# Kernel optimization log

Measured on AMD Instinct MI355X. Metric: run time of the kernel, lower is better.

## Reference

```python
import jax, jax.numpy as jnp
import numpy as np

DIM = 1024
NUM_HEADS = 16
HEAD_DIM = DIM // NUM_HEADS
ROPE_BASE = 10000.0


def _rope_cos_sin(seq_len, head_dim):
    inv_freq = 1.0 / (ROPE_BASE ** (jnp.arange(0, head_dim, 2, dtype=jnp.float32) / head_dim))
    t = jnp.arange(seq_len, dtype=jnp.float32)
    freqs = t[:, None] * inv_freq[None, :]            # [S, Dh/2]
    emb = jnp.concatenate([freqs, freqs], axis=-1)    # [S, Dh]
    return jnp.cos(emb), jnp.sin(emb)


def _rotate_half(x):
    half = x.shape[-1] // 2
    return jnp.concatenate([-x[..., half:], x[..., :half]], axis=-1)


def setup_inputs() -> dict:
    key = jax.random.key(0)
    k1, k2, k3 = jax.random.split(key, 3)
    B, S = 2, 2048
    x = jax.random.normal(k1, (B, S, DIM), dtype=jnp.float32)
    w_qkv = jax.random.normal(k2, (3 * DIM, DIM), dtype=jnp.float32) * (DIM ** -0.5)
    w_out = jax.random.normal(k3, (DIM, DIM), dtype=jnp.float32) * (DIM ** -0.5)
    return {"x": x, "w_qkv": w_qkv, "w_out": w_out}


def reference(x, w_qkv, w_out):
    B, S, D = x.shape
    H, Dh = NUM_HEADS, HEAD_DIM
    scale = Dh ** -0.5

    qkv = (x @ w_qkv.T).reshape(B, S, 3, H, Dh)      # [B,S,3,H,Dh]
    qkv = jnp.transpose(qkv, (2, 0, 3, 1, 4))        # [3,B,H,S,Dh]
    q, k, v = qkv[0], qkv[1], qkv[2]

    cos, sin = _rope_cos_sin(S, Dh)                  # [S,Dh]
    cos = cos[None, None, :, :]
    sin = sin[None, None, :, :]
    q = q * cos + _rotate_half(q) * sin
    k = k * cos + _rotate_half(k) * sin

    scores = jnp.einsum('bhqd,bhkd->bhqk', q, k) * scale
    causal_mask = jnp.triu(jnp.ones((S, S), dtype=bool), k=1)
    scores = jnp.where(causal_mask[None, None], -jnp.inf, scores)
    attn = jax.nn.softmax(scores, axis=-1)
    out = jnp.einsum('bhqk,bhkd->bhqd', attn, v)      # [B,H,S,Dh]
    out = jnp.transpose(out, (0, 2, 1, 3)).reshape(B, S, D)
    return out @ w_out.T
```

## Files before the change

kernel.cpp:

```cpp
#include <hip/hip_runtime.h>
#include <stdint.h>

typedef uint16_t u16;
typedef __attribute__((ext_vector_type(8))) short bf16x8;
typedef __attribute__((ext_vector_type(4))) float f32x4;

__device__ inline u16 f2b(float f) {
  uint32_t u = __float_as_uint(f);
  u += 0x7FFF + ((u >> 16) & 1);
  return (u16)(u >> 16);
}
__device__ inline float b2f(u16 h) {
  return __uint_as_float(((uint32_t)h) << 16);
}

typedef __attribute__((address_space(1))) void gvoid;
typedef __attribute__((address_space(3))) void lvoid;
#define GLOAD16(gp, lp)                                                        \
  __builtin_amdgcn_global_load_lds((gvoid*)(gp), (lvoid*)(lp), 16, 0, 0)

__device__ __forceinline__ int probe_mode(const u16* __restrict__ P, int t,
                                          int* cnt_sh) {
  if (t == 0) *cnt_sh = 0;
  __syncthreads();
  float av = fabsf(b2f(P[t * 2]));
  if (av >= 1000.0f) atomicAdd(cnt_sh, 1);
  __syncthreads();
  return (*cnt_sh > 16) ? 1 : 0;
}

__global__ __launch_bounds__(256) void k_qkv_rope(const void* __restrict__ Xv,
                                                  const void* __restrict__ Wv,
                                                  u16* __restrict__ Qo,
                                                  u16* __restrict__ Ko,
                                                  u16* __restrict__ Vo) {
  __shared__ u16 As[2][2][64][40];
  __shared__ u16 Bs[2][3][64][40];
  __shared__ float Cs[64][66];
  __shared__ int cnt_sh;
  const int t = threadIdx.x, w = t >> 6, lane = t & 63;
  const int mode = probe_mode((const u16*)Xv, t, &cnt_sh);
  const int h = blockIdx.x;
  const int n0h = h * 64;
  const int m0 = blockIdx.y * 128;
  const int lr = lane & 15, lq = lane >> 4;
  f32x4 acc[3][2][4] = {};
  const int rA = t >> 2, cA = (t & 3) * 8;
  const int aoff0 = (m0 + rA) * 1024 + cA;
  const int aoff1 = (m0 + 64 + rA) * 1024 + cA;
  const int boff0 = (n0h + rA) * 1024 + cA;

  if (mode == 0) {
    const u16* Xp = (const u16*)Xv;
    const u16* Wp = (const u16*)Wv;
    uint4 pa0 = *(const uint4*)(Xp + aoff0);
    uint4 pa1 = *(const uint4*)(Xp + aoff1);
    uint4 pb0 = *(const uint4*)(Wp + boff0);
    uint4 pb1 = *(const uint4*)(Wp + boff0 + 1048576);
    uint4 pb2 = *(const uint4*)(Wp + boff0 + 2097152);
    *(uint4*)&As[0][0][rA][cA] = pa0;
    *(uint4*)&As[0][1][rA][cA] = pa1;
    *(uint4*)&Bs[0][0][rA][cA] = pb0;
    *(uint4*)&Bs[0][1][rA][cA] = pb1;
    *(uint4*)&Bs[0][2][rA][cA] = pb2;
    pa0 = *(const uint4*)(Xp + aoff0 + 32);
    pa1 = *(const uint4*)(Xp + aoff1 + 32);
    pb0 = *(const uint4*)(Wp + boff0 + 32);
    pb1 = *(const uint4*)(Wp + boff0 + 1048576 + 32);
    pb2 = *(const uint4*)(Wp + boff0 + 2097152 + 32);
    __syncthreads();
    int cur = 0;
    for (int k0 = 0; k0 < 1024; k0 += 32) {
      if (k0 + 32 < 1024) {
        *(uint4*)&As[cur ^ 1][0][rA][cA] = pa0;
        *(uint4*)&As[cur ^ 1][1][rA][cA] = pa1;
        *(uint4*)&Bs[cur ^ 1][0][rA][cA] = pb0;
        *(uint4*)&Bs[cur ^ 1][1][rA][cA] = pb1;
        *(uint4*)&Bs[cur ^ 1][2][rA][cA] = pb2;
      }
      if (k0 + 64 < 1024) {
        const int kn = k0 + 64;
        pa0 = *(const uint4*)(Xp + aoff0 + kn);
        pa1 = *(const uint4*)(Xp + aoff1 + kn);
        pb0 = *(const uint4*)(Wp + boff0 + kn);
        pb1 = *(const uint4*)(Wp + boff0 + 1048576 + kn);
        pb2 = *(const uint4*)(Wp + boff0 + 2097152 + kn);
      }
      bf16x8 bf[3];
#pragma unroll
      for (int e = 0; e < 3; ++e)
        bf[e] = *(const bf16x8*)&Bs[cur][e][(w << 4) + lr][lq * 8];
#pragma unroll
      for (int mt = 0; mt < 4; ++mt) {
        bf16x8 af0 = *(const bf16x8*)&As[cur][0][(mt << 4) + lr][lq * 8];
        bf16x8 af1 = *(const bf16x8*)&As[cur][1][(mt << 4) + lr][lq * 8];
#pragma unroll
        for (int e = 0; e < 3; ++e) {
          acc[e][0][mt] = __builtin_amdgcn_mfma_f32_16x16x32_bf16(af0, bf[e], acc[e][0][mt], 0, 0, 0);
          acc[e][1][mt] = __builtin_amdgcn_mfma_f32_16x16x32_bf16(af1, bf[e], acc[e][1][mt], 0, 0, 0);
        }
      }
      __syncthreads();
      cur ^= 1;
    }
  } else {
    for (int k0 = 0; k0 < 1024; k0 += 32) {
      __syncthreads();
      const float* Xf = (const float*)Xv;
      const float* Wf = (const float*)Wv;
#pragma unroll
      for (int ee = 0; ee < 8; ++ee) {
        As[0][0][rA][cA + ee] = f2b(Xf[aoff0 + k0 + ee]);
        As[0][1][rA][cA + ee] = f2b(Xf[aoff1 + k0 + ee]);
        Bs[0][0][rA][cA + ee] = f2b(Wf[boff0 + k0 + ee]);
        Bs[0][1][rA][cA + ee] = f2b(Wf[boff0 + 1048576 + k0 + ee]);
        Bs[0][2][rA][cA + ee] = f2b(Wf[boff0 + 2097152 + k0 + ee]);
      }
      __syncthreads();
      bf16x8 bf[3];
#pragma unroll
      for (int e = 0; e < 3; ++e)
        bf[e] = *(const bf16x8*)&Bs[0][e][(w << 4) + lr][lq * 8];
#pragma unroll
      for (int mt = 0; mt < 4; ++mt) {
        bf16x8 af0 = *(const bf16x8*)&As[0][0][(mt << 4) + lr][lq * 8];
        bf16x8 af1 = *(const bf16x8*)&As[0][1][(mt << 4) + lr][lq * 8];
#pragma unroll
        for (int e = 0; e < 3; ++e) {
          acc[e][0][mt] = __builtin_amdgcn_mfma_f32_16x16x32_bf16(af0, bf[e], acc[e][0][mt], 0, 0, 0);
          acc[e][1][mt] = __builtin_amdgcn_mfma_f32_16x16x32_bf16(af1, bf[e], acc[e][1][mt], 0, 0, 0);
        }
      }
    }
  }

  for (int f = 0; f < 2; ++f) {
    const int m0f = m0 + f * 64;
    for (int e = 0; e < 3; ++e) {
      __syncthreads();
      {
        const int col = (w << 4) + lr;
#pragma unroll
        for (int mt = 0; mt < 4; ++mt)
#pragma unroll
          for (int i = 0; i < 4; ++i)
            Cs[mt * 16 + lq * 4 + i][col] = acc[e][f][mt][i];
      }
      __syncthreads();
      if (e == 2) {
        const int sx = t & 63, dh0 = (t >> 6) * 16;
        const int m = m0f + sx, b = m >> 11, s = m & 2047;
        const long hb = (long)(b * 16 + h) * 64;
#pragma unroll
        for (int u = 0; u < 16; ++u) {
          int dh = dh0 + u;
          Vo[(hb + dh) * 2048 + s] = f2b(Cs[sx][dh]);
        }
      } else {
        const int r = t >> 2, dh0 = (t & 3) * 16;
        const int m = m0f + r, b = m >> 11, s = m & 2047;
        const int obase = ((b * 16 + h) * 2048 + s) * 64;
        u16* O = (e == 0) ? Qo : Ko;
#pragma unroll
        for (int u = 0; u < 16; ++u) {
          int dh = dh0 + u;
          float v  = Cs[r][dh];
          float vp = Cs[r][dh ^ 32];
          float sign = (dh < 32) ? -1.0f : 1.0f;
          float fr  = __expf((float)(dh & 31) * -0.28782314f);
          float ang = (float)s * fr;
          float sn = __sinf(ang), cs = __cosf(ang);
          O[obase + dh] = f2b(v * cs + sign * vp * sn);
        }
      }
    }
  }
}

__device__ __forceinline__ void attn_tile(u16 QP[64][72], u16 Ks[64][72],
                                          u16 Vt[64][72], const bf16x8 qf[2],
                                          f32x4 o_acc[4], float& m_i, float& l_i,
                                          int kt, int qt_tile, int w, int lr,
                                          int lq, int lq4, int base16, int qrow_l) {
  f32x4 sa[4] = {};
#pragma unroll
  for (int mb = 0; mb < 4; ++mb)
#pragma unroll
    for (int kk = 0; kk < 2; ++kk) {
      bf16x8 kf = *(const bf16x8*)&Ks[mb * 16 + lr][kk * 32 + lq * 8];
      sa[mb] = __builtin_amdgcn_mfma_f32_16x16x32_bf16(kf, qf[kk], sa[mb], 0, 0, 0);
    }
  float sc[4][4];
  float m_new = m_i;
#pragma unroll
  for (int mb = 0; mb < 4; ++mb)
#pragma unroll
    for (int i = 0; i < 4; ++i) {
      float sv = sa[mb][i] * 0.125f;
      if (kt == qt_tile && (mb * 16 + lq4 + i) > qrow_l) sv = -3.0e4f;
      sc[mb][i] = sv;
      m_new = fmaxf(m_new, sv);
    }
  m_new = fmaxf(m_new, __shfl_xor(m_new, 16));
  m_new = fmaxf(m_new, __shfl_xor(m_new, 32));
  float alpha = __expf(m_i - m_new);
  m_i = m_new;
  float p[4][4], sm = 0.f;
#pragma unroll
  for (int mb = 0; mb < 4; ++mb)
#pragma unroll
    for (int i = 0; i < 4; ++i) { p[mb][i] = __expf(sc[mb][i] - m_new); sm += p[mb][i]; }
  sm += __shfl_xor(sm, 16);
  sm += __shfl_xor(sm, 32);
  l_i = l_i * alpha + sm;
#pragma unroll
  for (int mb = 0; mb < 4; ++mb) {
    uint2 pk;
    pk.x = (uint32_t)f2b(p[mb][0]) | ((uint32_t)f2b(p[mb][1]) << 16);
    pk.y = (uint32_t)f2b(p[mb][2]) | ((uint32_t)f2b(p[mb][3]) << 16);
    *(uint2*)&QP[w * 16 + lr][mb * 16 + lq4] = pk;
  }
#pragma unroll
  for (int i = 0; i < 4; ++i) {
    float ai = __shfl(alpha, base16 | (lq4 + i));
    o_acc[0][i] *= ai; o_acc[1][i] *= ai;
    o_acc[2][i] *= ai; o_acc[3][i] *= ai;
  }
  asm volatile("s_waitcnt lgkmcnt(0)" ::: "memory");
#pragma unroll
  for (int kk = 0; kk < 2; ++kk) {
    bf16x8 pf = *(const bf16x8*)&QP[w * 16 + lr][kk * 32 + lq * 8];
#pragma unroll
    for (int nb = 0; nb < 4; ++nb) {
      bf16x8 vf = *(const bf16x8*)&Vt[nb * 16 + lr][kk * 32 + lq * 8];
      o_acc[nb] = __builtin_amdgcn_mfma_f32_16x16x32_bf16(pf, vf, o_acc[nb], 0, 0, 0);
    }
  }
}

__global__ __launch_bounds__(256) void k_attn(const u16* __restrict__ Q,
                                              const u16* __restrict__ K,
                                              const u16* __restrict__ V,
                                              u16* __restrict__ AO) {
  __shared__ u16 QP[64][72];
  __shared__ u16 Ks[2][64][72];
  __shared__ u16 Vt[2][64][72];
  const int qtA = 31 - blockIdx.x;
  const int qtB = blockIdx.x;
  const int bh = blockIdx.y;
  const int b = bh >> 4, h = bh & 15;
  const u16* Qg = Q + (bh * 2048) * 64;
  const u16* Kg = K + bh * 2048 * 64;
  const u16* Vg = V + (long)bh * 64 * 2048;
  const int t = threadIdx.x, w = t >> 6, lane = t & 63;
  const int lr = lane & 15, lq = lane >> 4;
  const int lq4 = lq * 4;
  const int base16 = lane & 48;
  const int r0 = t >> 3, c0 = (t & 7) * 8;
  const int qrow_l = w * 16 + lr;

  uint4 pk0 = *(const uint4*)&Kg[r0 * 64 + c0];
  uint4 pk1 = *(const uint4*)&Kg[(r0 + 32) * 64 + c0];
  uint4 pv0 = *(const uint4*)&Vg[r0 * 2048 + c0];
  uint4 pv1 = *(const uint4*)&Vg[(r0 + 32) * 2048 + c0];

  bf16x8 qfA[2], qfB[2];
  *(uint4*)&QP[r0][c0]      = *(const uint4*)&Qg[(qtA * 64 + r0) * 64 + c0];
  *(uint4*)&QP[r0 + 32][c0] = *(const uint4*)&Qg[(qtA * 64 + r0 + 32) * 64 + c0];
  __syncthreads();
#pragma unroll
  for (int kk = 0; kk < 2; ++kk)
    qfA[kk] = *(const bf16x8*)&QP[w * 16 + lr][kk * 32 + lq * 8];
  __syncthreads();
  *(uint4*)&QP[r0][c0]      = *(const uint4*)&Qg[(qtB * 64 + r0) * 64 + c0];
  *(uint4*)&QP[r0 + 32][c0] = *(const uint4*)&Qg[(qtB * 64 + r0 + 32) * 64 + c0];
  __syncthreads();
#pragma unroll
  for (int kk = 0; kk < 2; ++kk)
    qfB[kk] = *(const bf16x8*)&QP[w * 16 + lr][kk * 32 + lq * 8];

  *(uint4*)&Ks[0][r0][c0]      = pk0;
  *(uint4*)&Ks[0][r0 + 32][c0] = pk1;
  *(uint4*)&Vt[0][r0][c0]      = pv0;
  *(uint4*)&Vt[0][r0 + 32][c0] = pv1;
  pk0 = *(const uint4*)&Kg[(64 + r0) * 64 + c0];
  pk1 = *(const uint4*)&Kg[(64 + r0 + 32) * 64 + c0];
  pv0 = *(const uint4*)&Vg[r0 * 2048 + 64 + c0];
  pv1 = *(const uint4*)&Vg[(r0 + 32) * 2048 + 64 + c0];
  __syncthreads();

  float m_iA = -3.0e4f, l_iA = 0.f, m_iB = -3.0e4f, l_iB = 0.f;
  f32x4 o_accA[4] = {}, o_accB[4] = {};

  int cur = 0;
  for (int kt = 0; kt <= qtA; ++kt) {
    if (kt + 1 <= qtA) {
      *(uint4*)&Ks[cur ^ 1][r0][c0]      = pk0;
      *(uint4*)&Ks[cur ^ 1][r0 + 32][c0] = pk1;
      *(uint4*)&Vt[cur ^ 1][r0][c0]      = pv0;
      *(uint4*)&Vt[cur ^ 1][r0 + 32][c0] = pv1;
    }
    if (kt + 2 <= qtA) {
      const int kn = kt + 2;
      pk0 = *(const uint4*)&Kg[(kn * 64 + r0) * 64 + c0];
      pk1 = *(const uint4*)&Kg[(kn * 64 + r0 + 32) * 64 + c0];
      pv0 = *(const uint4*)&Vg[r0 * 2048 + kn * 64 + c0];
      pv1 = *(const uint4*)&Vg[(r0 + 32) * 2048 + kn * 64 + c0];
    }

    attn_tile(QP, Ks[cur], Vt[cur], qfA, o_accA, m_iA, l_iA, kt, qtA,
              w, lr, lq, lq4, base16, qrow_l);
    if (kt <= qtB) {
      asm volatile("s_waitcnt lgkmcnt(0)" ::: "memory");
      attn_tile(QP, Ks[cur], Vt[cur], qfB, o_accB, m_iB, l_iB, kt, qtB,
                w, lr, lq, lq4, base16, qrow_l);
    }
    __syncthreads();
    cur ^= 1;
  }
  float linvA = 1.0f / l_iA, linvB = 1.0f / l_iB;
#pragma unroll
  for (int i = 0; i < 4; ++i) {
    float invA = __shfl(linvA, base16 | (lq4 + i));
    float invB = __shfl(linvB, base16 | (lq4 + i));
    int rowA = qtA * 64 + w * 16 + lq4 + i;
    int rowB = qtB * 64 + w * 16 + lq4 + i;
    int obA = (b * 2048 + rowA) * 1024 + h * 64;
    int obB = (b * 2048 + rowB) * 1024 + h * 64;
#pragma unroll
    for (int nb = 0; nb < 4; ++nb) {
      AO[obA + nb * 16 + lr] = f2b(o_accA[nb][i] * invA);
      AO[obB + nb * 16 + lr] = f2b(o_accB[nb][i] * invB);
    }
  }
}

__global__ __launch_bounds__(256) void k_gemm_out(const u16* __restrict__ A,
                                                  const void* __restrict__ Bv,
                                                  void* __restrict__ Cv) {
  __shared__ u16 As[2][64][32];
  __shared__ u16 Bs[2][2][64][32];
  __shared__ int cnt_sh;
  const int t = threadIdx.x, w = t >> 6, lane = t & 63;
  const int mode = probe_mode((const u16*)Bv, t, &cnt_sh);
  const int n0 = blockIdx.x * 128, m0 = blockIdx.y * 64;
  const int lr = lane & 15, lq = lane >> 4;
  f32x4 acc[2][4] = {};
  const int rA = t >> 2;
  const int gcol = (((t & 3) ^ ((rA >> 1) & 3)) << 3);
  const int aoff  = (m0 + rA) * 1024 + gcol;
  const int boff0 = (n0 + rA) * 1024 + gcol;
  const int boff1 = boff0 + 65536;

  if (mode == 0) {
    const u16* Bp = (const u16*)Bv;
#define STAGE_OUT(buf, kk)                                                     \
    do {                                                                       \
      GLOAD16(A + aoff + (kk),   &As[buf][(w << 4)][0]);                       \
      GLOAD16(Bp + boff0 + (kk), &Bs[buf][0][(w << 4)][0]);                    \
      GLOAD16(Bp + boff1 + (kk), &Bs[buf][1][(w << 4)][0]);                    \
    } while (0)
    STAGE_OUT(0, 0);
    asm volatile("s_waitcnt vmcnt(0)" ::: "memory");
    __syncthreads();
    int cur = 0;
    for (int k0 = 0; k0 < 1024; k0 += 32) {
      if (k0 + 32 < 1024) STAGE_OUT(cur ^ 1, k0 + 32);
      bf16x8 bfx[2];
      const int rowB = (w << 4) + lr;
      const int scB = ((lq ^ ((rowB >> 1) & 3)) << 3);
#pragma unroll
      for (int e = 0; e < 2; ++e)
        bfx[e] = *(const bf16x8*)&Bs[cur][e][rowB][scB];
#pragma unroll
      for (int mt = 0; mt < 4; ++mt) {
        const int row = (mt << 4) + lr;
        const int sc = ((lq ^ ((row >> 1) & 3)) << 3);
        bf16x8 af = *(const bf16x8*)&As[cur][row][sc];
#pragma unroll
        for (int e = 0; e < 2; ++e)
          acc[e][mt] = __builtin_amdgcn_mfma_f32_16x16x32_bf16(af, bfx[e], acc[e][mt], 0, 0, 0);
      }
      __syncthreads();
      cur ^= 1;
    }
#undef STAGE_OUT
  } else {
    const float* Bf = (const float*)Bv;
    for (int k0 = 0; k0 < 1024; k0 += 32) {
      __syncthreads();
      *(uint4*)&As[0][rA][(t & 3) << 3] = *(const uint4*)(A + (m0 + rA) * 1024 + ((t & 3) << 3) + k0);
#pragma unroll
      for (int ee = 0; ee < 8; ++ee) {
        const int pc = ((t & 3) << 3) + ee;
        Bs[0][0][rA][pc] = f2b(Bf[(n0 + rA) * 1024 + pc + k0]);
        Bs[0][1][rA][pc] = f2b(Bf[(n0 + rA) * 1024 + 65536 + pc + k0]);
      }
      __syncthreads();
      bf16x8 bfx[2];
      const int rowB = (w << 4) + lr;
#pragma unroll
      for (int e = 0; e < 2; ++e)
        bfx[e] = *(const bf16x8*)&Bs[0][e][rowB][lq * 8];
#pragma unroll
      for (int mt = 0; mt < 4; ++mt) {
        bf16x8 af = *(const bf16x8*)&As[0][(mt << 4) + lr][lq * 8];
#pragma unroll
        for (int e = 0; e < 2; ++e)
          acc[e][mt] = __builtin_amdgcn_mfma_f32_16x16x32_bf16(af, bfx[e], acc[e][mt], 0, 0, 0);
      }
    }
  }
#pragma unroll
  for (int e = 0; e < 2; ++e) {
    const int col = n0 + e * 64 + (w << 4) + lr;
    if (mode == 0) {
      u16* C = (u16*)Cv;
#pragma unroll
      for (int mt = 0; mt < 4; ++mt)
#pragma unroll
        for (int i = 0; i < 4; ++i)
          C[(m0 + mt * 16 + lq * 4 + i) * 1024 + col] = f2b(acc[e][mt][i]);
    } else {
      float* C = (float*)Cv;
#pragma unroll
      for (int mt = 0; mt < 4; ++mt)
#pragma unroll
        for (int i = 0; i < 4; ++i)
          C[(m0 + mt * 16 + lq * 4 + i) * 1024 + col] = acc[e][mt][i];
    }
  }
}

extern "C" void kernel_launch(void* const* d_in, const int* in_sizes, int n_in,
                              void* d_out, int out_size, void* d_ws, size_t ws_size,
                              hipStream_t stream) {
  const void* x    = d_in[0];
  const void* wqkv = d_in[1];
  const void* wout = d_in[2];

  u16* qb = (u16*)((char*)d_ws + 256);
  u16* kb = qb + 4194304;
  u16* vb = kb + 4194304;
  u16* ao = vb + 4194304;

  k_qkv_rope<<<dim3(16, 32), 256, 0, stream>>>(x, wqkv, qb, kb, vb);
  k_attn    <<<dim3(16, 32), 256, 0, stream>>>(qb, kb, vb, ao);
  k_gemm_out<<<dim3(8, 64), 256, 0, stream>>>(ao, wout, d_out);
}
```

Before: 218.3 us.

## Retile QKV GEMM to 128x128 blocks with direct-to-LDS loads and register RoPE

The QKV projection kernel now tiles the output as 128x128 blocks over a 2x2 wave grid, one of Q, K or V per block, instead of one head's 64 columns across all three projections. Operand tiles go straight into LDS through global_load_lds with an XOR swizzle, replacing register staging and manual double buffering. RoPE for Q and K is applied directly from the accumulators, pairing nt with nt^2, so the LDS round-trip disappears for Q and K. The goals are better operand reuse per block and fewer LDS stores, at the cost of losing software prefetch overlap, since each k-step now uses two barriers and a single buffer.

```diff
diff --git a/kernel.cpp b/kernel.cpp
--- a/kernel.cpp
+++ b/kernel.cpp
@@ -34,144 +34,133 @@
                                                   u16* __restrict__ Qo,
                                                   u16* __restrict__ Ko,
                                                   u16* __restrict__ Vo) {
-  __shared__ u16 As[2][2][64][40];
-  __shared__ u16 Bs[2][3][64][40];
-  __shared__ float Cs[64][66];
+  union Sh {
+    struct { u16 A[128][32]; u16 B[128][32]; } st;
+    float Cs[64][66];
+  };
+  __shared__ Sh sh;
   __shared__ int cnt_sh;
   const int t = threadIdx.x, w = t >> 6, lane = t & 63;
   const int mode = probe_mode((const u16*)Xv, t, &cnt_sh);
-  const int h = blockIdx.x;
-  const int n0h = h * 64;
+  const int e  = blockIdx.x >> 3;
+  const int nb = blockIdx.x & 7;
+  const int n0 = nb * 128;
   const int m0 = blockIdx.y * 128;
   const int lr = lane & 15, lq = lane >> 4;
-  f32x4 acc[3][2][4] = {};
-  const int rA = t >> 2, cA = (t & 3) * 8;
-  const int aoff0 = (m0 + rA) * 1024 + cA;
-  const int aoff1 = (m0 + 64 + rA) * 1024 + cA;
-  const int boff0 = (n0h + rA) * 1024 + cA;
+  const int wm = w >> 1, wn = w & 1;
+  f32x4 acc[4][4] = {};
 
   if (mode == 0) {
     const u16* Xp = (const u16*)Xv;
     const u16* Wp = (const u16*)Wv;
-    uint4 pa0 = *(const uint4*)(Xp + aoff0);
-    uint4 pa1 = *(const uint4*)(Xp + aoff1);
-    uint4 pb0 = *(const uint4*)(Wp + boff0);
-    uint4 pb1 = *(const uint4*)(Wp + boff0 + 1048576);
-    uint4 pb2 = *(const uint4*)(Wp + boff0 + 2097152);
-    *(uint4*)&As[0][0][rA][cA] = pa0;
-    *(uint4*)&As[0][1][rA][cA] = pa1;
-    *(uint4*)&Bs[0][0][rA][cA] = pb0;
-    *(uint4*)&Bs[0][1][rA][cA] = pb1;
-    *(uint4*)&Bs[0][2][rA][cA] = pb2;
-    pa0 = *(const uint4*)(Xp + aoff0 + 32);
-    pa1 = *(const uint4*)(Xp + aoff1 + 32);
-    pb0 = *(const uint4*)(Wp + boff0 + 32);
-    pb1 = *(const uint4*)(Wp + boff0 + 1048576 + 32);
-    pb2 = *(const uint4*)(Wp + boff0 + 2097152 + 32);
-    __syncthreads();
-    int cur = 0;
+    const int lrow = lane >> 2;
+    const int lg   = (lane & 3) ^ (lrow & 3);
+    const int arow = m0 + w * 32 + lrow;
+    const int brow = e * 1024 + n0 + w * 32 + lrow;
+    const u16* asrc0 = Xp + (long)arow * 1024 + lg * 8;
+    const u16* asrc1 = Xp + (long)(arow + 16) * 1024 + lg * 8;
+    const u16* bsrc0 = Wp + (long)brow * 1024 + lg * 8;
+    const u16* bsrc1 = Wp + (long)(brow + 16) * 1024 + lg * 8;
+    u16* ad0 = &sh.st.A[w * 32][0];
+    u16* ad1 = &sh.st.A[w * 32 + 16][0];
+    u16* bd0 = &sh.st.B[w * 32][0];
+    u16* bd1 = &sh.st.B[w * 32 + 16][0];
     for (int k0 = 0; k0 < 1024; k0 += 32) {
-      if (k0 + 32 < 1024) {
-        *(uint4*)&As[cur ^ 1][0][rA][cA] = pa0;
-        *(uint4*)&As[cur ^ 1][1][rA][cA] = pa1;
-        *(uint4*)&Bs[cur ^ 1][0][rA][cA] = pb0;
-        *(uint4*)&Bs[cur ^ 1][1][rA][cA] = pb1;
-        *(uint4*)&Bs[cur ^ 1][2][rA][cA] = pb2;
-      }
-      if (k0 + 64 < 1024) {
-        const int kn = k0 + 64;
-        pa0 = *(const uint4*)(Xp + aoff0 + kn);
-        pa1 = *(const uint4*)(Xp + aoff1 + kn);
-        pb0 = *(const uint4*)(Wp + boff0 + kn);
-        pb1 = *(const uint4*)(Wp + boff0 + 1048576 + kn);
-        pb2 = *(const uint4*)(Wp + boff0 + 2097152 + kn);
-      }
-      bf16x8 bf[3];
-#pragma unroll
-      for (int e = 0; e < 3; ++e)
-        bf[e] = *(const bf16x8*)&Bs[cur][e][(w << 4) + lr][lq * 8];
-#pragma unroll
-      for (int mt = 0; mt < 4; ++mt) {
-        bf16x8 af0 = *(const bf16x8*)&As[cur][0][(mt << 4) + lr][lq * 8];
-        bf16x8 af1 = *(const bf16x8*)&As[cur][1][(mt << 4) + lr][lq * 8];
-#pragma unroll
-        for (int e = 0; e < 3; ++e) {
-          acc[e][0][mt] = __builtin_amdgcn_mfma_f32_16x16x32_bf16(af0, bf[e], acc[e][0][mt], 0, 0, 0);
-          acc[e][1][mt] = __builtin_amdgcn_mfma_f32_16x16x32_bf16(af1, bf[e], acc[e][1][mt], 0, 0, 0);
+      __syncthreads();
+      GLOAD16(asrc0 + k0, ad0);
+      GLOAD16(asrc1 + k0, ad1);
+      GLOAD16(bsrc0 + k0, bd0);
+      GLOAD16(bsrc1 + k0, bd1);
+      __syncthreads();
+      bf16x8 af[4], bf[4];
+#pragma unroll
+      for (int x = 0; x < 4; ++x) {
+        const int ra = wm * 64 + x * 16 + lr;
+        const int rb = wn * 64 + x * 16 + lr;
+        af[x] = *(const bf16x8*)&sh.st.A[ra][(lq ^ (lr & 3)) * 8];
+        bf[x] = *(const bf16x8*)&sh.st.B[rb][(lq ^ (lr & 3)) * 8];
+      }
+#pragma unroll
+      for (int mt = 0; mt < 4; ++mt)
+#pragma unroll
+        for (int nt = 0; nt < 4; ++nt)
+          acc[mt][nt] = __builtin_amdgcn_mfma_f32_16x16x32_bf16(af[mt], bf[nt], acc[mt][nt], 0, 0, 0);
+    }
+  } else {
+    const float* Xf = (const float*)Xv;
+    const float* Wf = (const float*)Wv;
+    const int r = t >> 1, ch = (t & 1) * 16;
+    for (int k0 = 0; k0 < 1024; k0 += 32) {
+      __syncthreads();
+#pragma unroll
+      for (int j = 0; j < 16; ++j) {
+        sh.st.A[r][ch + j] = f2b(Xf[(long)(m0 + r) * 1024 + k0 + ch + j]);
+        sh.st.B[r][ch + j] = f2b(Wf[(long)(e * 1024 + n0 + r) * 1024 + k0 + ch + j]);
+      }
+      __syncthreads();
+      bf16x8 af[4], bf[4];
+#pragma unroll
+      for (int x = 0; x < 4; ++x) {
+        af[x] = *(const bf16x8*)&sh.st.A[wm * 64 + x * 16 + lr][lq * 8];
+        bf[x] = *(const bf16x8*)&sh.st.B[wn * 64 + x * 16 + lr][lq * 8];
+      }
+#pragma unroll
+      for (int mt = 0; mt < 4; ++mt)
+#pragma unroll
+        for (int nt = 0; nt < 4; ++nt)
+          acc[mt][nt] = __builtin_amdgcn_mfma_f32_16x16x32_bf16(af[mt], bf[nt], acc[mt][nt], 0, 0, 0);
+    }
+  }
+
+  if (e < 2) {
+    u16* O = (e == 0) ? Qo : Ko;
+    const float fr0 = __expf((float)lr * -0.28782314f);
+    const float fr1 = __expf((float)(16 + lr) * -0.28782314f);
+#pragma unroll
+    for (int mt = 0; mt < 4; ++mt)
+#pragma unroll
+      for (int i = 0; i < 4; ++i) {
+        const int m = m0 + wm * 64 + mt * 16 + lq * 4 + i;
+        const int b = m >> 11, s = m & 2047;
+        float sn0, cs0, sn1, cs1;
+        __sincosf((float)s * fr0, &sn0, &cs0);
+        __sincosf((float)s * fr1, &sn1, &cs1);
+#pragma unroll
+        for (int nt = 0; nt < 4; ++nt) {
+          const int ng = n0 + wn * 64 + nt * 16 + lr;
+          const int h = ng >> 6, dh = ng & 63;
+          const float v  = acc[mt][nt][i];
+          const float vp = acc[mt][nt ^ 2][i];
+          const float sn = (nt & 1) ? sn1 : sn0;
+          const float cs = (nt & 1) ? cs1 : cs0;
+          const float sign = (dh < 32) ? -1.0f : 1.0f;
+          O[((long)(b * 16 + h) * 2048 + s) * 64 + dh] = f2b(v * cs + sign * vp * sn);
         }
       }
-      __syncthreads();
-      cur ^= 1;
-    }
   } else {
-    for (int k0 = 0; k0 < 1024; k0 += 32) {
-      __syncthreads();
-      const float* Xf = (const float*)Xv;
-      const float* Wf = (const float*)Wv;
-#pragma unroll
-      for (int ee = 0; ee < 8; ++ee) {
-        As[0][0][rA][cA + ee] = f2b(Xf[aoff0 + k0 + ee]);
-        As[0][1][rA][cA + ee] = f2b(Xf[aoff1 + k0 + ee]);
-        Bs[0][0][rA][cA + ee] = f2b(Wf[boff0 + k0 + ee]);
-        Bs[0][1][rA][cA + ee] = f2b(Wf[boff0 + 1048576 + k0 + ee]);
-        Bs[0][2][rA][cA + ee] = f2b(Wf[boff0 + 2097152 + k0 + ee]);
-      }
-      __syncthreads();
-      bf16x8 bf[3];
-#pragma unroll
-      for (int e = 0; e < 3; ++e)
-        bf[e] = *(const bf16x8*)&Bs[0][e][(w << 4) + lr][lq * 8];
-#pragma unroll
-      for (int mt = 0; mt < 4; ++mt) {
-        bf16x8 af0 = *(const bf16x8*)&As[0][0][(mt << 4) + lr][lq * 8];
-        bf16x8 af1 = *(const bf16x8*)&As[0][1][(mt << 4) + lr][lq * 8];
-#pragma unroll
-        for (int e = 0; e < 3; ++e) {
-          acc[e][0][mt] = __builtin_amdgcn_mfma_f32_16x16x32_bf16(af0, bf[e], acc[e][0][mt], 0, 0, 0);
-          acc[e][1][mt] = __builtin_amdgcn_mfma_f32_16x16x32_bf16(af1, bf[e], acc[e][1][mt], 0, 0, 0);
-        }
-      }
-    }
-  }
-
-  for (int f = 0; f < 2; ++f) {
-    const int m0f = m0 + f * 64;
-    for (int e = 0; e < 3; ++e) {
-      __syncthreads();
-      {
-        const int col = (w << 4) + lr;
+#pragma unroll 1
+    for (int q = 0; q < 4; ++q) {
+      const int qm = q >> 1, qn = q & 1;
+      __syncthreads();
+      if (wm == qm && wn == qn) {
 #pragma unroll
         for (int mt = 0; mt < 4; ++mt)
 #pragma unroll
           for (int i = 0; i < 4; ++i)
-            Cs[mt * 16 + lq * 4 + i][col] = acc[e][f][mt][i];
-      }
-      __syncthreads();
-      if (e == 2) {
-        const int sx = t & 63, dh0 = (t >> 6) * 16;
-        const int m = m0f + sx, b = m >> 11, s = m & 2047;
-        const long hb = (long)(b * 16 + h) * 64;
-#pragma unroll
-        for (int u = 0; u < 16; ++u) {
-          int dh = dh0 + u;
-          Vo[(hb + dh) * 2048 + s] = f2b(Cs[sx][dh]);
-        }
-      } else {
-        const int r = t >> 2, dh0 = (t & 3) * 16;
-        const int m = m0f + r, b = m >> 11, s = m & 2047;
-        const int obase = ((b * 16 + h) * 2048 + s) * 64;
-        u16* O = (e == 0) ? Qo : Ko;
-#pragma unroll
-        for (int u = 0; u < 16; ++u) {
-          int dh = dh0 + u;
-          float v  = Cs[r][dh];
-          float vp = Cs[r][dh ^ 32];
-          float sign = (dh < 32) ? -1.0f : 1.0f;
-          float fr  = __expf((float)(dh & 31) * -0.28782314f);
-          float ang = (float)s * fr;
-          float sn = __sinf(ang), cs = __cosf(ang);
-          O[obase + dh] = f2b(v * cs + sign * vp * sn);
-        }
+#pragma unroll
+            for (int nt = 0; nt < 4; ++nt)
+              sh.Cs[mt * 16 + lq * 4 + i][nt * 16 + lr] = acc[mt][nt][i];
+      }
+      __syncthreads();
+      const int sx = t & 63, dh0 = (t >> 6) * 16;
+      const int mlin = m0 + qm * 64 + sx;
+      const int b = mlin >> 11, s = mlin & 2047;
+#pragma unroll
+      for (int u = 0; u < 16; ++u) {
+        const int dl = dh0 + u;
+        const int ng = n0 + qn * 64 + dl;
+        const int h = ng >> 6, dh = ng & 63;
+        Vo[((long)(b * 16 + h) * 64 + dh) * 2048 + s] = f2b(sh.Cs[sx][dl]);
       }
     }
   }
@@ -444,7 +433,7 @@
   u16* vb = kb + 4194304;
   u16* ao = vb + 4194304;
 
-  k_qkv_rope<<<dim3(16, 32), 256, 0, stream>>>(x, wqkv, qb, kb, vb);
+  k_qkv_rope<<<dim3(24, 32), 256, 0, stream>>>(x, wqkv, qb, kb, vb);
   k_attn    <<<dim3(16, 32), 256, 0, stream>>>(qb, kb, vb, ao);
   k_gemm_out<<<dim3(8, 64), 256, 0, stream>>>(ao, wout, d_out);
 }
```

Result: slower. 327.7 us (+50.1%).

## Single-buffer K/V, split attention tile into stages, interleave two query tiles

Applied to the files above, without the earlier changes.

Splits the per-tile attention into QK, softmax and PV stages so the second query tile's QK MFMAs can be issued between the first tile's softmax and PV, with a separate P buffer for tile B. K/V staging in LDS drops from double to single buffering, with two barriers per iteration and a prefetch distance of one tile instead of two. Launch bounds now request 4 blocks per CU to raise occupancy. The cost is less latency hiding for the global K/V loads and an extra barrier per iteration, traded for lower LDS use and better MFMA/VALU overlap.

```diff
diff --git a/kernel.cpp b/kernel.cpp
--- a/kernel.cpp
+++ b/kernel.cpp
@@ -177,19 +177,23 @@
   }
 }
 
-__device__ __forceinline__ void attn_tile(u16 QP[64][72], u16 Ks[64][72],
-                                          u16 Vt[64][72], const bf16x8 qf[2],
-                                          f32x4 o_acc[4], float& m_i, float& l_i,
-                                          int kt, int qt_tile, int w, int lr,
-                                          int lq, int lq4, int base16, int qrow_l) {
-  f32x4 sa[4] = {};
-#pragma unroll
-  for (int mb = 0; mb < 4; ++mb)
+__device__ __forceinline__ void qk_tile(const u16 Ks[64][72], const bf16x8 qf[2],
+                                        f32x4 sa[4], int lr, int lq) {
+#pragma unroll
+  for (int mb = 0; mb < 4; ++mb) {
+    sa[mb] = (f32x4){0.f, 0.f, 0.f, 0.f};
 #pragma unroll
     for (int kk = 0; kk < 2; ++kk) {
       bf16x8 kf = *(const bf16x8*)&Ks[mb * 16 + lr][kk * 32 + lq * 8];
       sa[mb] = __builtin_amdgcn_mfma_f32_16x16x32_bf16(kf, qf[kk], sa[mb], 0, 0, 0);
     }
+  }
+}
+
+__device__ __forceinline__ void softmax_tile(const f32x4 sa[4], u16 P[64][72],
+                                             f32x4 o_acc[4], float& m_i, float& l_i,
+                                             int kt, int qt_tile, int w, int lr,
+                                             int lq4, int base16, int qrow_l) {
   float sc[4][4];
   float m_new = m_i;
 #pragma unroll
@@ -218,7 +222,7 @@
     uint2 pk;
     pk.x = (uint32_t)f2b(p[mb][0]) | ((uint32_t)f2b(p[mb][1]) << 16);
     pk.y = (uint32_t)f2b(p[mb][2]) | ((uint32_t)f2b(p[mb][3]) << 16);
-    *(uint2*)&QP[w * 16 + lr][mb * 16 + lq4] = pk;
+    *(uint2*)&P[w * 16 + lr][mb * 16 + lq4] = pk;
   }
 #pragma unroll
   for (int i = 0; i < 4; ++i) {
@@ -226,10 +230,14 @@
     o_acc[0][i] *= ai; o_acc[1][i] *= ai;
     o_acc[2][i] *= ai; o_acc[3][i] *= ai;
   }
+}
+
+__device__ __forceinline__ void pv_tile(const u16 P[64][72], const u16 Vt[64][72],
+                                        f32x4 o_acc[4], int w, int lr, int lq) {
   asm volatile("s_waitcnt lgkmcnt(0)" ::: "memory");
 #pragma unroll
   for (int kk = 0; kk < 2; ++kk) {
-    bf16x8 pf = *(const bf16x8*)&QP[w * 16 + lr][kk * 32 + lq * 8];
+    bf16x8 pf = *(const bf16x8*)&P[w * 16 + lr][kk * 32 + lq * 8];
 #pragma unroll
     for (int nb = 0; nb < 4; ++nb) {
       bf16x8 vf = *(const bf16x8*)&Vt[nb * 16 + lr][kk * 32 + lq * 8];
@@ -238,13 +246,14 @@
   }
 }
 
-__global__ __launch_bounds__(256) void k_attn(const u16* __restrict__ Q,
-                                              const u16* __restrict__ K,
-                                              const u16* __restrict__ V,
-                                              u16* __restrict__ AO) {
+__global__ __launch_bounds__(256, 4) void k_attn(const u16* __restrict__ Q,
+                                                 const u16* __restrict__ K,
+                                                 const u16* __restrict__ V,
+                                                 u16* __restrict__ AO) {
   __shared__ u16 QP[64][72];
-  __shared__ u16 Ks[2][64][72];
-  __shared__ u16 Vt[2][64][72];
+  __shared__ u16 PB[64][72];
+  __shared__ u16 Ks[64][72];
+  __shared__ u16 Vt[64][72];
   const int qtA = 31 - blockIdx.x;
   const int qtB = blockIdx.x;
   const int bh = blockIdx.y;
@@ -279,44 +288,34 @@
   for (int kk = 0; kk < 2; ++kk)
     qfB[kk] = *(const bf16x8*)&QP[w * 16 + lr][kk * 32 + lq * 8];
 
-  *(uint4*)&Ks[0][r0][c0]      = pk0;
-  *(uint4*)&Ks[0][r0 + 32][c0] = pk1;
-  *(uint4*)&Vt[0][r0][c0]      = pv0;
-  *(uint4*)&Vt[0][r0 + 32][c0] = pv1;
-  pk0 = *(const uint4*)&Kg[(64 + r0) * 64 + c0];
-  pk1 = *(const uint4*)&Kg[(64 + r0 + 32) * 64 + c0];
-  pv0 = *(const uint4*)&Vg[r0 * 2048 + 64 + c0];
-  pv1 = *(const uint4*)&Vg[(r0 + 32) * 2048 + 64 + c0];
-  __syncthreads();
-
   float m_iA = -3.0e4f, l_iA = 0.f, m_iB = -3.0e4f, l_iB = 0.f;
   f32x4 o_accA[4] = {}, o_accB[4] = {};
 
-  int cur = 0;
   for (int kt = 0; kt <= qtA; ++kt) {
-    if (kt + 1 <= qtA) {
-      *(uint4*)&Ks[cur ^ 1][r0][c0]      = pk0;
-      *(uint4*)&Ks[cur ^ 1][r0 + 32][c0] = pk1;
-      *(uint4*)&Vt[cur ^ 1][r0][c0]      = pv0;
-      *(uint4*)&Vt[cur ^ 1][r0 + 32][c0] = pv1;
-    }
-    if (kt + 2 <= qtA) {
-      const int kn = kt + 2;
+    __syncthreads();
+    *(uint4*)&Ks[r0][c0]      = pk0;
+    *(uint4*)&Ks[r0 + 32][c0] = pk1;
+    *(uint4*)&Vt[r0][c0]      = pv0;
+    *(uint4*)&Vt[r0 + 32][c0] = pv1;
+    __syncthreads();
+    if (kt < qtA) {
+      const int kn = kt + 1;
       pk0 = *(const uint4*)&Kg[(kn * 64 + r0) * 64 + c0];
       pk1 = *(const uint4*)&Kg[(kn * 64 + r0 + 32) * 64 + c0];
       pv0 = *(const uint4*)&Vg[r0 * 2048 + kn * 64 + c0];
       pv1 = *(const uint4*)&Vg[(r0 + 32) * 2048 + kn * 64 + c0];
     }
 
-    attn_tile(QP, Ks[cur], Vt[cur], qfA, o_accA, m_iA, l_iA, kt, qtA,
-              w, lr, lq, lq4, base16, qrow_l);
-    if (kt <= qtB) {
-      asm volatile("s_waitcnt lgkmcnt(0)" ::: "memory");
-      attn_tile(QP, Ks[cur], Vt[cur], qfB, o_accB, m_iB, l_iB, kt, qtB,
-                w, lr, lq, lq4, base16, qrow_l);
-    }
-    __syncthreads();
-    cur ^= 1;
+    const bool doB = (kt <= qtB);
+    f32x4 sa[4];
+    qk_tile(Ks, qfA, sa, lr, lq);
+    softmax_tile(sa, QP, o_accA, m_iA, l_iA, kt, qtA, w, lr, lq4, base16, qrow_l);
+    if (doB) qk_tile(Ks, qfB, sa, lr, lq);
+    pv_tile(QP, Vt, o_accA, w, lr, lq);
+    if (doB) {
+      softmax_tile(sa, PB, o_accB, m_iB, l_iB, kt, qtB, w, lr, lq4, base16, qrow_l);
+      pv_tile(PB, Vt, o_accB, w, lr, lq);
+    }
   }
   float linvA = 1.0f / l_iA, linvB = 1.0f / l_iB;
 #pragma unroll
```

Measured after the change: 300.7 us. +37.7%, slower.
